# Performance work log

Hardware: AMD Instinct MI355X
Metric: run time of the kernel (lower is better)

Reference implementation:

```python
import jax, jax.numpy as jnp
import numpy as np

HEADS = 16
HEAD_DIM = 1024 // HEADS  # 64
SCALE = float(np.sqrt(HEAD_DIM))  # math.sqrt(features // heads)


def setup_inputs() -> dict:
    key = jax.random.key(0)
    ks = jax.random.split(key, 6)
    n, m, d, c = 2048, 2048, 1024, 768
    return {
        "x": jax.random.normal(ks[0], (n, d), dtype=jnp.float32),
        "ctx": jax.random.normal(ks[1], (m, c), dtype=jnp.float32),
        "Wq": jax.random.normal(ks[2], (d, d), dtype=jnp.float32) * (1.0 / np.sqrt(d)),
        "Wk": jax.random.normal(ks[3], (c, d), dtype=jnp.float32) * (1.0 / np.sqrt(c)),
        "Wv": jax.random.normal(ks[4], (c, d), dtype=jnp.float32) * (1.0 / np.sqrt(c)),
        "Wo": jax.random.normal(ks[5], (d, d), dtype=jnp.float32) * (1.0 / np.sqrt(d)),
    }


def reference(x, ctx, Wq, Wk, Wv, Wo):
    n, d = x.shape
    q = (x @ Wq).reshape(n, HEADS, HEAD_DIM).transpose(1, 0, 2)      # h n d
    k = (ctx @ Wk).reshape(-1, HEADS, HEAD_DIM).transpose(1, 0, 2)   # h m d
    v = (ctx @ Wv).reshape(-1, HEADS, HEAD_DIM).transpose(1, 0, 2)   # h m d
    scores = jnp.einsum("hnd,hmd->hnm", q, k) / SCALE
    attn = jax.nn.softmax(scores, axis=-1)
    out = jnp.einsum("hnm,hmd->hnd", attn, v)                        # h n d
    out = out.transpose(1, 0, 2).reshape(n, d)                       # n (h d)
    return out @ Wo
```

## Files before the change

### kernel.cpp

```cpp
#include <hip/hip_runtime.h>
#include <hip/hip_bf16.h>
#include <stdint.h>

typedef unsigned short bfu;
typedef __attribute__((ext_vector_type(8))) short short8;
typedef __attribute__((ext_vector_type(4))) float f32x4;

__device__ __forceinline__ bfu f2bf(float f) {
  union { float f; uint32_t u; } v; v.f = f;
  uint32_t r = (v.u + 0x7fffu + ((v.u >> 16) & 1u)) >> 16;
  return (bfu)r;
}

__device__ __forceinline__ void gload16(const void* g, void* l) {
  __builtin_amdgcn_global_load_lds((const __attribute__((address_space(1))) void*)g,
                                   (__attribute__((address_space(3))) void*)l, 16, 0, 0);
}

__global__ __launch_bounds__(256) void conv_kernel(const float* __restrict__ in,
                                                   bfu* __restrict__ out, int n8) {
  int i = blockIdx.x * blockDim.x + threadIdx.x;
  if (i >= n8) return;
  const float4* p = (const float4*)in + (size_t)i * 2;
  float4 a = p[0], b = p[1];
  union { bfu h[8]; uint4 v; } o;
  o.h[0] = f2bf(a.x); o.h[1] = f2bf(a.y); o.h[2] = f2bf(a.z); o.h[3] = f2bf(a.w);
  o.h[4] = f2bf(b.x); o.h[5] = f2bf(b.y); o.h[6] = f2bf(b.z); o.h[7] = f2bf(b.w);
  ((uint4*)out)[i] = o.v;
}

__device__ __forceinline__ void trans_body(const float* __restrict__ W, bfu* __restrict__ WT,
                                           int Kd, int n0, int k0) {
  __shared__ float tile[32][33];
  const int tx = threadIdx.x & 31, ty = threadIdx.x >> 5;
#pragma unroll
  for (int i = 0; i < 32; i += 8)
    tile[ty + i][tx] = W[(size_t)(k0 + ty + i) * 1024 + n0 + tx];
  __syncthreads();
#pragma unroll
  for (int i = 0; i < 32; i += 8)
    WT[(size_t)(n0 + ty + i) * Kd + k0 + tx] = f2bf(tile[tx][ty + i]);
}

__global__ __launch_bounds__(256) void trans4_kernel(
    const float* __restrict__ Wq, const float* __restrict__ Wk,
    const float* __restrict__ Wv, const float* __restrict__ Wo,
    bfu* WTq, bfu* WTk, bfu* WTv, bfu* WTo) {
  int b = blockIdx.x;
  if (b < 1024)       trans_body(Wq, WTq, 1024, (b & 31) * 32, (b >> 5) * 32);
  else if (b < 1792) { b -= 1024; trans_body(Wk, WTk, 768, (b & 31) * 32, (b >> 5) * 32); }
  else if (b < 2560) { b -= 1792; trans_body(Wv, WTv, 768, (b & 31) * 32, (b >> 5) * 32); }
  else               { b -= 2560; trans_body(Wo, WTo, 1024, (b & 31) * 32, (b >> 5) * 32); }
}

typedef bfu AsArr[2][4][128][8];
typedef bfu BsArr[2][4][64][8];

__device__ __forceinline__ void gemm_body(AsArr& As2, BsArr& Bs2,
    const bfu* __restrict__ A, const bfu* __restrict__ BT,
    bfu* __restrict__ Cb, float* __restrict__ Cf,
    int N, int K, float scale, int m0, int n0) {
  const int tid = threadIdx.x, lane = tid & 63, wave = tid >> 6;
  const int g = lane >> 4, c = lane & 15;
  const int wm = wave * 32;
  const int nt = K / 32;

  auto stage = [&](int buf, int kt) {
#pragma unroll
    for (int u = 0; u < 3; ++u) {
      int idx = wave * 3 + u;
      if (idx < 8) {
        int g2 = idx & 3, rb = idx >> 2;
        gload16(&A[(size_t)(m0 + rb * 64 + lane) * K + kt + g2 * 8], &As2[buf][g2][rb * 64][0]);
      } else {
        int g2 = idx - 8;
        gload16(&BT[(size_t)(n0 + lane) * K + kt + g2 * 8], &Bs2[buf][g2][0][0]);
      }
    }
  };

  f32x4 acc[2][4] = {};
  stage(0, 0);
  for (int t = 0; t < nt; ++t) {
    __syncthreads();
    if (t + 1 < nt) stage((t + 1) & 1, (t + 1) * 32);
    const int b = t & 1;
    short8 af[2], bfr[4];
#pragma unroll
    for (int i = 0; i < 2; ++i) af[i] = *(const short8*)&As2[b][g][wm + i * 16 + c][0];
#pragma unroll
    for (int j = 0; j < 4; ++j) bfr[j] = *(const short8*)&Bs2[b][g][j * 16 + c][0];
#pragma unroll
    for (int i = 0; i < 2; ++i)
#pragma unroll
      for (int j = 0; j < 4; ++j)
        acc[i][j] = __builtin_amdgcn_mfma_f32_16x16x32_bf16(af[i], bfr[j], acc[i][j], 0, 0, 0);
  }
#pragma unroll
  for (int i = 0; i < 2; ++i)
#pragma unroll
    for (int j = 0; j < 4; ++j) {
      int row = m0 + wm + i * 16 + g * 4;
      int col = n0 + j * 16 + c;
#pragma unroll
      for (int r = 0; r < 4; ++r) {
        float v = acc[i][j][r] * scale;
        if (Cb) Cb[(size_t)(row + r) * N + col] = f2bf(v);
        else    Cf[(size_t)(row + r) * N + col] = v;
      }
    }
}

__global__ __launch_bounds__(256) void gemm3_kernel(
    const bfu* __restrict__ xb, const bfu* __restrict__ WTq, bfu* __restrict__ Qb,
    const bfu* __restrict__ ctxb, const bfu* __restrict__ WTk, bfu* __restrict__ Kb,
    const bfu* __restrict__ WTv, bfu* __restrict__ Vtb) {
  __shared__ alignas(16) bfu As2[2][4][128][8];
  __shared__ alignas(16) bfu Bs2[2][4][64][8];
  int bid = blockIdx.x, p = bid >> 8, r = bid & 255;
  if (p == 0)
    gemm_body(As2, Bs2, xb, WTq, Qb, nullptr, 1024, 1024, 0.125f, (r >> 4) * 128, (r & 15) * 64);
  else if (p == 1)
    gemm_body(As2, Bs2, ctxb, WTk, Kb, nullptr, 1024, 768, 1.0f, (r >> 4) * 128, (r & 15) * 64);
  else
    gemm_body(As2, Bs2, WTv, ctxb, Vtb, nullptr, 2048, 768, 1.0f, (r >> 5) * 128, (r & 31) * 64);
}

__global__ __launch_bounds__(256) void gemmo_kernel(const bfu* __restrict__ AO,
                                                    const bfu* __restrict__ WTo,
                                                    float* __restrict__ out) {
  __shared__ alignas(16) bfu As2[2][4][128][8];
  __shared__ alignas(16) bfu Bs2[2][4][64][8];
  int bid = blockIdx.x;
  gemm_body(As2, Bs2, AO, WTo, nullptr, out, 1024, 1024, 1.0f, (bid >> 4) * 128, (bid & 15) * 64);
}

__global__ __launch_bounds__(256) void attn_kernel(
    const bfu* __restrict__ Q, const bfu* __restrict__ Kmat,
    const bfu* __restrict__ Vt, bfu* __restrict__ O) {
  __shared__ alignas(16) bfu Ks[2][8][64][8];
  __shared__ alignas(16) bfu Vs[2][8][64][8];
  __shared__ alignas(16) bfu Ps[4][16][72];
  const int tid = threadIdx.x, wave = tid >> 6, lane = tid & 63;
  const int g = lane >> 4, c = lane & 15;
  const int h = blockIdx.y;
  const int q0 = blockIdx.x * 64 + wave * 16;
  const int col0 = h * 64;

  short8 qf0 = *(const short8*)&Q[(size_t)(q0 + c) * 1024 + col0 + g * 8];
  short8 qf1 = *(const short8*)&Q[(size_t)(q0 + c) * 1024 + col0 + 32 + g * 8];

  short8 ones;
#pragma unroll
  for (int e = 0; e < 8; ++e) ones[e] = (short)0x3F80;

  f32x4 o_acc[4] = {};
  f32x4 lacc = {};

  auto stage = [&](int buf, int kv0) {
#pragma unroll
    for (int u = 0; u < 4; ++u) {
      int idx = wave * 4 + u;
      if (idx < 8)
        gload16(&Kmat[(size_t)(kv0 + lane) * 1024 + col0 + idx * 8], &Ks[buf][idx][0][0]);
      else
        gload16(&Vt[(size_t)(col0 + lane) * 2048 + kv0 + (idx - 8) * 8], &Vs[buf][idx - 8][0][0]);
    }
  };

  stage(0, 0);
  for (int t = 0; t < 32; ++t) {
    __syncthreads();
    if (t < 31) stage((t + 1) & 1, (t + 1) * 64);
    const int b = t & 1;
    f32x4 s[4] = {};
    __builtin_amdgcn_s_setprio(1);
#pragma unroll
    for (int f = 0; f < 4; ++f) {
      short8 kf0 = *(const short8*)&Ks[b][g][f * 16 + c][0];
      short8 kf1 = *(const short8*)&Ks[b][4 + g][f * 16 + c][0];
      s[f] = __builtin_amdgcn_mfma_f32_16x16x32_bf16(qf0, kf0, s[f], 0, 0, 0);
      s[f] = __builtin_amdgcn_mfma_f32_16x16x32_bf16(qf1, kf1, s[f], 0, 0, 0);
    }
    __builtin_amdgcn_s_setprio(0);
#pragma unroll
    for (int f = 0; f < 4; ++f)
#pragma unroll
      for (int j = 0; j < 4; ++j)
        Ps[wave][g * 4 + j][f * 16 + c] = f2bf(__expf(s[f][j]));
    __syncthreads();
    __builtin_amdgcn_s_setprio(1);
#pragma unroll
    for (int kc = 0; kc < 2; ++kc) {
      short8 pf = *(const short8*)&Ps[wave][c][kc * 32 + g * 8];
      lacc = __builtin_amdgcn_mfma_f32_16x16x32_bf16(pf, ones, lacc, 0, 0, 0);
#pragma unroll
      for (int fd = 0; fd < 4; ++fd) {
        short8 vf = *(const short8*)&Vs[b][kc * 4 + g][fd * 16 + c][0];
        o_acc[fd] = __builtin_amdgcn_mfma_f32_16x16x32_bf16(pf, vf, o_acc[fd], 0, 0, 0);
      }
    }
    __builtin_amdgcn_s_setprio(0);
  }
#pragma unroll
  for (int fd = 0; fd < 4; ++fd)
#pragma unroll
    for (int j = 0; j < 4; ++j) {
      float v = o_acc[fd][j] / lacc[j];
      O[(size_t)(q0 + g * 4 + j) * 1024 + col0 + fd * 16 + c] = f2bf(v);
    }
}

extern "C" void kernel_launch(void* const* d_in, const int* in_sizes, int n_in,
                              void* d_out, int out_size, void* d_ws, size_t ws_size,
                              hipStream_t stream) {
  const float* x   = (const float*)d_in[0];
  const float* ctx = (const float*)d_in[1];
  const float* Wq  = (const float*)d_in[2];
  const float* Wk  = (const float*)d_in[3];
  const float* Wv  = (const float*)d_in[4];
  const float* Wo  = (const float*)d_in[5];
  float* out = (float*)d_out;

  bfu* ws   = (bfu*)d_ws;
  bfu* xb   = ws;
  bfu* WTk  = xb + 2048 * 1024;
  bfu* WTv  = WTk + 1024 * 768;
  bfu* WTo  = WTv + 1024 * 768;
  bfu* Qb   = WTo + 1024 * 1024;
  bfu* Kb   = Qb + 2048 * 1024;
  bfu* Vtb  = Kb + 2048 * 1024;
  bfu* WTq  = (bfu*)d_out;
  bfu* ctxb = WTq + 1024 * 1024;

  dim3 blk(256);
  conv_kernel<<<1024, blk, 0, stream>>>(x, xb, 2048 * 1024 / 8);
  conv_kernel<<<768, blk, 0, stream>>>(ctx, ctxb, 2048 * 768 / 8);
  trans4_kernel<<<3584, blk, 0, stream>>>(Wq, Wk, Wv, Wo, WTq, WTk, WTv, WTo);
  gemm3_kernel<<<768, blk, 0, stream>>>(xb, WTq, Qb, ctxb, WTk, Kb, WTv, Vtb);
  attn_kernel<<<dim3(32, 16), blk, 0, stream>>>(Qb, Kb, Vtb, xb);
  gemmo_kernel<<<256, blk, 0, stream>>>(xb, WTo, out);
}
```

Before: 120.1 us.

## Triple-buffer attention K/V loads and merge conversion kernels into one prep launch

```diff
diff --git a/kernel.cpp b/kernel.cpp
--- a/kernel.cpp
+++ b/kernel.cpp
@@ -17,10 +17,8 @@
                                    (__attribute__((address_space(3))) void*)l, 16, 0, 0);
 }
 
-__global__ __launch_bounds__(256) void conv_kernel(const float* __restrict__ in,
-                                                   bfu* __restrict__ out, int n8) {
-  int i = blockIdx.x * blockDim.x + threadIdx.x;
-  if (i >= n8) return;
+__device__ __forceinline__ void conv_body(const float* __restrict__ in, bfu* __restrict__ out,
+                                          int i) {
   const float4* p = (const float4*)in + (size_t)i * 2;
   float4 a = p[0], b = p[1];
   union { bfu h[8]; uint4 v; } o;
@@ -42,15 +40,18 @@
     WT[(size_t)(n0 + ty + i) * Kd + k0 + tx] = f2bf(tile[tx][ty + i]);
 }
 
-__global__ __launch_bounds__(256) void trans4_kernel(
+__global__ __launch_bounds__(256) void prep_kernel(
+    const float* __restrict__ x, const float* __restrict__ ctx,
     const float* __restrict__ Wq, const float* __restrict__ Wk,
     const float* __restrict__ Wv, const float* __restrict__ Wo,
-    bfu* WTq, bfu* WTk, bfu* WTv, bfu* WTo) {
+    bfu* xb, bfu* ctxb, bfu* WTq, bfu* WTk, bfu* WTv, bfu* WTo) {
   int b = blockIdx.x;
-  if (b < 1024)       trans_body(Wq, WTq, 1024, (b & 31) * 32, (b >> 5) * 32);
-  else if (b < 1792) { b -= 1024; trans_body(Wk, WTk, 768, (b & 31) * 32, (b >> 5) * 32); }
-  else if (b < 2560) { b -= 1792; trans_body(Wv, WTv, 768, (b & 31) * 32, (b >> 5) * 32); }
-  else               { b -= 2560; trans_body(Wo, WTo, 1024, (b & 31) * 32, (b >> 5) * 32); }
+  if (b < 1024)       conv_body(x, xb, b * 256 + threadIdx.x);
+  else if (b < 1792)  conv_body(ctx, ctxb, (b - 1024) * 256 + threadIdx.x);
+  else if (b < 2816) { b -= 1792; trans_body(Wq, WTq, 1024, (b & 31) * 32, (b >> 5) * 32); }
+  else if (b < 3584) { b -= 2816; trans_body(Wk, WTk, 768, (b & 31) * 32, (b >> 5) * 32); }
+  else if (b < 4352) { b -= 3584; trans_body(Wv, WTv, 768, (b & 31) * 32, (b >> 5) * 32); }
+  else               { b -= 4352; trans_body(Wo, WTo, 1024, (b & 31) * 32, (b >> 5) * 32); }
 }
 
 typedef bfu AsArr[2][4][128][8];
@@ -138,8 +139,8 @@
 __global__ __launch_bounds__(256) void attn_kernel(
     const bfu* __restrict__ Q, const bfu* __restrict__ Kmat,
     const bfu* __restrict__ Vt, bfu* __restrict__ O) {
-  __shared__ alignas(16) bfu Ks[2][8][64][8];
-  __shared__ alignas(16) bfu Vs[2][8][64][8];
+  __shared__ alignas(16) bfu Ks[3][8][64][8];
+  __shared__ alignas(16) bfu Vs[3][8][64][8];
   __shared__ alignas(16) bfu Ps[4][16][72];
   const int tid = threadIdx.x, wave = tid >> 6, lane = tid & 63;
   const int g = lane >> 4, c = lane & 15;
@@ -169,10 +170,11 @@
   };
 
   stage(0, 0);
+  stage(1, 64);
   for (int t = 0; t < 32; ++t) {
-    __syncthreads();
-    if (t < 31) stage((t + 1) & 1, (t + 1) * 64);
-    const int b = t & 1;
+    const int b = t % 3;
+    asm volatile("s_waitcnt vmcnt(4) lgkmcnt(0)\n\ts_barrier" ::: "memory");
+    __builtin_amdgcn_sched_barrier(0);
     f32x4 s[4] = {};
     __builtin_amdgcn_s_setprio(1);
 #pragma unroll
@@ -188,7 +190,9 @@
 #pragma unroll
       for (int j = 0; j < 4; ++j)
         Ps[wave][g * 4 + j][f * 16 + c] = f2bf(__expf(s[f][j]));
-    __syncthreads();
+    asm volatile("s_waitcnt lgkmcnt(0)\n\ts_barrier" ::: "memory");
+    __builtin_amdgcn_sched_barrier(0);
+    { int tn = t + 2; stage(tn % 3, (tn & 31) * 64); }
     __builtin_amdgcn_s_setprio(1);
 #pragma unroll
     for (int kc = 0; kc < 2; ++kc) {
@@ -234,9 +238,7 @@
   bfu* ctxb = WTq + 1024 * 1024;
 
   dim3 blk(256);
-  conv_kernel<<<1024, blk, 0, stream>>>(x, xb, 2048 * 1024 / 8);
-  conv_kernel<<<768, blk, 0, stream>>>(ctx, ctxb, 2048 * 768 / 8);
-  trans4_kernel<<<3584, blk, 0, stream>>>(Wq, Wk, Wv, Wo, WTq, WTk, WTv, WTo);
+  prep_kernel<<<5376, blk, 0, stream>>>(x, ctx, Wq, Wk, Wv, Wo, xb, ctxb, WTq, WTk, WTv, WTo);
   gemm3_kernel<<<768, blk, 0, stream>>>(xb, WTq, Qb, ctxb, WTk, Kb, WTv, Vtb);
   attn_kernel<<<dim3(32, 16), blk, 0, stream>>>(Qb, Kb, Vtb, xb);
   gemmo_kernel<<<256, blk, 0, stream>>>(xb, WTo, out);
```

After: 117.4 us. 2.3% less time.
